# Optimization experiments

Measured on AMD Instinct MI355X. Metric: run time of the kernel, lower is better.

Reference implementation:

```python
import jax, jax.numpy as jnp
import numpy as np

B, N, D_IN, D_HID, D_OUT = 8, 512, 4608, 4608, 1152
DROP = 0.1
INV_SQRT2 = 0.7071067811865476
INV_SQRT_2PI = 0.3989422804014327


def _clean(s):
    # nan -> 1e-5, inf -> 1.0 (matches torch.where chain)
    return jnp.where(jnp.isnan(s), jnp.asarray(1e-5, s.dtype),
                     jnp.where(jnp.isinf(s), jnp.asarray(1.0, s.dtype), s))


def kl_regularizer(w_mu, w_sigma):
    d = w_mu.shape[0]
    ws = jax.nn.softplus(w_sigma)  # log(1+exp(w_sigma))
    return 0.5 * jnp.mean(d * ws + jnp.sum(w_mu * w_mu, axis=0) - d - d * jnp.log(ws))


def vdp_linear(mu_in, Sigma_in, w_mu, w_sigma):
    mu_out = jnp.matmul(mu_in, w_mu)                                 # [B,N,U]
    kl = kl_regularizer(w_mu, w_sigma)
    W_Sigma = jax.nn.softplus(w_sigma)                               # [U]
    Sigma_1 = jnp.matmul(Sigma_in, w_mu * w_mu)                      # w^T Sigma_in w (diag)
    Sigma_2 = jnp.sum(mu_in * mu_in, axis=-1, keepdims=True) * W_Sigma
    Sigma_3 = jnp.sum(Sigma_in, axis=-1, keepdims=True) * W_Sigma
    return mu_out, _clean(Sigma_1 + Sigma_2 + Sigma_3), kl


def vdp_gelu(mu_in, Sigma_in):
    # exact (erf) gelu and its analytic derivative: Phi(x) + x*phi(x)
    cdf = 0.5 * (1.0 + jax.lax.erf(mu_in * INV_SQRT2))
    pdf = jnp.exp(-0.5 * mu_in * mu_in) * INV_SQRT_2PI
    grad = cdf + mu_in * pdf
    return mu_in * cdf, grad * grad * Sigma_in


def vdp_dropout(mu_in, Sigma_in, mask):
    keep = 1.0 - DROP
    m = mask.astype(mu_in.dtype)
    mu_out = mu_in * m / keep                       # torch F.dropout scaling
    Sigma_out = Sigma_in * m / mu_in.shape[-1]      # kept Sigma values (unscaled), / units
    return mu_out, _clean(Sigma_out)


def setup_inputs() -> dict:
    key = jax.random.key(0)
    k = jax.random.split(key, 8)
    mu_in = jax.random.normal(k[0], (B, N, D_IN), dtype=jnp.float32)
    sigma_in = jax.random.uniform(k[1], (B, N, D_IN), dtype=jnp.float32)
    mask1 = jax.random.bernoulli(k[2], 1.0 - DROP, (B, N, D_HID))
    mask2 = jax.random.bernoulli(k[3], 1.0 - DROP, (B, N, D_OUT))
    w_mu1 = 0.05 * jax.random.normal(k[4], (D_IN, D_HID), dtype=jnp.float32)
    w_sigma1 = jnp.full((D_HID,), -4.6, dtype=jnp.float32)
    w_mu2 = 0.05 * jax.random.normal(k[5], (D_HID, D_OUT), dtype=jnp.float32)
    w_sigma2 = jnp.full((D_OUT,), -4.6, dtype=jnp.float32)
    return {"mu_in": mu_in, "sigma_in": sigma_in, "mask1": mask1, "mask2": mask2,
            "w_mu1": w_mu1, "w_sigma1": w_sigma1, "w_mu2": w_mu2, "w_sigma2": w_sigma2}


def reference(mu_in, sigma_in, mask1, mask2, w_mu1, w_sigma1, w_mu2, w_sigma2):
    mu, sig, kl1 = vdp_linear(mu_in, sigma_in, w_mu1, w_sigma1)
    mu, sig = vdp_gelu(mu, sig)
    mu, sig = vdp_dropout(mu, sig, mask1)
    mu, sig, kl2 = vdp_linear(mu, sig, w_mu2, w_sigma2)
    mu, sig = vdp_dropout(mu, sig, mask2)
    return mu, _clean(sig), kl1 + kl2
```

## Files before the change

### kernel.cpp

```cpp
#include <hip/hip_runtime.h>
#include <cstdint>
#include <cstddef>

static constexpr int Mrows = 4096;
static constexpr int K1 = 4608;
static constexpr int N1 = 4608;
static constexpr int N2 = 1152;
static constexpr int SPLITK = 2;
static constexpr int NPART1 = (K1 / 32) * (N1 / 32);
static constexpr int NPART2 = (K1 / 32) * (N2 / 32);

static constexpr float SC_WSQ   = 4096.f;
static constexpr float SC_SIG3  = 16384.f;
static constexpr float DSC_L2   = 1.f / (SC_SIG3 * SC_WSQ);

typedef float  f32x4  __attribute__((ext_vector_type(4)));
typedef __bf16 bf16x8 __attribute__((ext_vector_type(8)));

__device__ __forceinline__ unsigned short f2bf(float f) {
  unsigned int u = __float_as_uint(f);
  u += 0x7fffu + ((u >> 16) & 1u);
  return (unsigned short)(u >> 16);
}
__device__ __forceinline__ float bf2f(unsigned short h) {
  return __uint_as_float(((unsigned int)h) << 16);
}
__device__ __forceinline__ float cleanf(float s) {
  if (__builtin_isnan(s)) return 1e-5f;
  if (__builtin_isinf(s)) return 1.0f;
  return s;
}
__device__ __forceinline__ unsigned int pk_fp8x4(float a, float b, float c, float d) {
  int p = __builtin_amdgcn_cvt_pk_fp8_f32(a, b, 0, false);
  p = __builtin_amdgcn_cvt_pk_fp8_f32(c, d, p, true);
  return (unsigned int)p;
}

__global__ __launch_bounds__(256) void prep_in(
    const float* __restrict__ mu, const float* __restrict__ sg,
    unsigned short* __restrict__ A1, unsigned short* __restrict__ As16,
    float* __restrict__ rmu2, float* __restrict__ rsg)
{
  const int row = blockIdx.x;
  const int tid = threadIdx.x;
  const float4* mup = (const float4*)(mu + (size_t)row * K1);
  const float4* sgp = (const float4*)(sg + (size_t)row * K1);
  ushort4* a1p = (ushort4*)(A1 + (size_t)row * K1);
  ushort4* asp = (ushort4*)(As16 + (size_t)row * K1);
  float smu = 0.f, ssg = 0.f;
  for (int j = tid; j < K1 / 4; j += 256) {
    float4 m4 = mup[j];
    float4 s4 = sgp[j];
    smu += m4.x*m4.x + m4.y*m4.y + m4.z*m4.z + m4.w*m4.w;
    ssg += s4.x + s4.y + s4.z + s4.w;
    a1p[j] = make_ushort4(f2bf(m4.x), f2bf(m4.y), f2bf(m4.z), f2bf(m4.w));
    asp[j] = make_ushort4(f2bf(s4.x), f2bf(s4.y), f2bf(s4.z), f2bf(s4.w));
  }
  __shared__ float red[2][4];
  for (int off = 32; off; off >>= 1) {
    smu += __shfl_down(smu, off);
    ssg += __shfl_down(ssg, off);
  }
  const int lane = tid & 63, wv = tid >> 6;
  if (!lane) { red[0][wv] = smu; red[1][wv] = ssg; }
  __syncthreads();
  if (tid == 0) {
    rmu2[row] = red[0][0] + red[0][1] + red[0][2] + red[0][3];
    rsg[row]  = red[1][0] + red[1][1] + red[1][2] + red[1][3];
  }
}

__global__ __launch_bounds__(256) void prep_w(
    const float* __restrict__ w, unsigned short* __restrict__ Bt,
    void* __restrict__ Bsq, float* __restrict__ partials,
    int K, int N, int sq16)
{
  __shared__ float t[32][33];
  const int kt = blockIdx.x * 32;
  const int nt = blockIdx.y * 32;
  const int tx = threadIdx.x & 31;
  const int ty = threadIdx.x >> 5;
  float loc = 0.f;
#pragma unroll
  for (int i = 0; i < 32; i += 8) {
    float v = w[(size_t)(kt + ty + i) * N + (nt + tx)];
    t[ty + i][tx] = v;
    loc += v * v;
  }
  __syncthreads();
#pragma unroll
  for (int i = 0; i < 32; i += 8) {
    float v = t[tx][ty + i];
    size_t o = (size_t)(nt + ty + i) * K + (kt + tx);
    Bt[o] = f2bf(v);
    if (sq16)
      ((unsigned short*)Bsq)[o] = f2bf(v * v);
    else
      ((unsigned char*)Bsq)[o] =
          (unsigned char)(__builtin_amdgcn_cvt_pk_fp8_f32(v * v * SC_WSQ, 0.f, 0, false) & 0xff);
  }
  __shared__ float red[4];
  for (int off = 32; off; off >>= 1) loc += __shfl_down(loc, off);
  const int lane = threadIdx.x & 63, wv = threadIdx.x >> 6;
  if (!lane) red[wv] = loc;
  __syncthreads();
  if (threadIdx.x == 0)
    partials[blockIdx.y * gridDim.x + blockIdx.x] = red[0] + red[1] + red[2] + red[3];
}

__global__ __launch_bounds__(256) void kl_prep(
    const float* __restrict__ wsig1, const float* __restrict__ wsig2,
    const float* __restrict__ part1, const float* __restrict__ part2,
    float* __restrict__ ws1, float* __restrict__ ws2, float* __restrict__ outkl)
{
  const int tid = threadIdx.x;
  float s1 = 0.f, l1 = 0.f, s2 = 0.f, l2 = 0.f, q1 = 0.f, q2 = 0.f;
  for (int j = tid; j < N1; j += 256) {
    float x = wsig1[j];
    float sp = (x > 20.f) ? x : log1pf(expf(x));
    ws1[j] = sp; s1 += sp; l1 += logf(sp);
  }
  for (int j = tid; j < N2; j += 256) {
    float x = wsig2[j];
    float sp = (x > 20.f) ? x : log1pf(expf(x));
    ws2[j] = sp; s2 += sp; l2 += logf(sp);
  }
  for (int j = tid; j < NPART1; j += 256) q1 += part1[j];
  for (int j = tid; j < NPART2; j += 256) q2 += part2[j];
  __shared__ float red[6][4];
  for (int off = 32; off; off >>= 1) {
    s1 += __shfl_down(s1, off); l1 += __shfl_down(l1, off);
    s2 += __shfl_down(s2, off); l2 += __shfl_down(l2, off);
    q1 += __shfl_down(q1, off); q2 += __shfl_down(q2, off);
  }
  const int lane = tid & 63, wv = tid >> 6;
  if (!lane) {
    red[0][wv] = s1; red[1][wv] = l1; red[2][wv] = s2;
    red[3][wv] = l2; red[4][wv] = q1; red[5][wv] = q2;
  }
  __syncthreads();
  if (tid == 0) {
    float S1v = red[0][0] + red[0][1] + red[0][2] + red[0][3];
    float L1v = red[1][0] + red[1][1] + red[1][2] + red[1][3];
    float S2v = red[2][0] + red[2][1] + red[2][2] + red[2][3];
    float L2v = red[3][0] + red[3][1] + red[3][2] + red[3][3];
    float Q1v = red[4][0] + red[4][1] + red[4][2] + red[4][3];
    float Q2v = red[5][0] + red[5][1] + red[5][2] + red[5][3];
    const float d = 4608.f;
    float kl1 = 0.5f * (d * (S1v / (float)N1) + Q1v / (float)N1 - d - d * (L1v / (float)N1));
    float kl2 = 0.5f * (d * (S2v / (float)N2) + Q2v / (float)N2 - d - d * (L2v / (float)N2));
    outkl[0] = kl1 + kl2;
  }
}

#define GLD16(gp, lp) __builtin_amdgcn_global_load_lds( \
    (__attribute__((address_space(1))) void*)(unsigned short*)(gp), \
    (__attribute__((address_space(3))) void*)(lp), 16, 0, 0)

__global__ __launch_bounds__(512, 2) void gemm256(
    const unsigned short* __restrict__ Amu, const unsigned short* __restrict__ Asg,
    const unsigned short* __restrict__ Bmu, const unsigned short* __restrict__ Bsq,
    unsigned short* __restrict__ Cmu, unsigned short* __restrict__ Csg)
{
  __shared__ __align__(16) char smem[114688];
  char* lA = smem;
  char* lB = smem + 65536;

  const int tid  = threadIdx.x;
  const int lane = tid & 63;
  const int wave = tid >> 6;
  const int which = blockIdx.z;
  const unsigned short* Ag = which ? Asg : Amu;
  const unsigned short* Bg = which ? Bsq : Bmu;
  unsigned short* Cg = which ? Csg : Cmu;

  const int m0 = blockIdx.y * 256;
  const int n0 = blockIdx.x * 192;
  const int wm = (wave >> 2) * 128;
  const int wn = (wave & 3) * 48;
  const int fm = lane & 15;
  const int kq = lane >> 4;

  const int rbase = tid >> 3;
  const int gg = (tid & 7) ^ (rbase & 7);
  const unsigned short* gA0 = Ag + (size_t)(m0 + rbase) * K1 + gg * 8;
  const unsigned short* gB0 = Bg + (size_t)(n0 + rbase) * K1 + gg * 8;

  auto stA = [&](int buf, int h, int kt2) {
    const unsigned short* g = gA0 + (size_t)h * 128 * K1 + (size_t)kt2 * 64;
    char* l = lA + buf * 32768 + h * 16384 + tid * 16;
    GLD16(g, l);
    GLD16(g + (size_t)64 * K1, l + 8192);
  };
  auto stB = [&](int buf, int kt2) {
    const unsigned short* g = gB0 + (size_t)kt2 * 64;
    char* l = lB + buf * 24576 + tid * 16;
    GLD16(g, l);
    GLD16(g + (size_t)64 * K1, l + 8192);
    GLD16(g + (size_t)128 * K1, l + 16384);
  };

  const int abase = (wm + fm) * 128;
  const int bbase = 65536 + (wn + fm) * 128;
  const int x0 = ((0 * 4 + kq) ^ (fm & 7)) * 16;
  const int x1 = ((1 * 4 + kq) ^ (fm & 7)) * 16;

  f32x4 acc[8][3];
#pragma unroll
  for (int i = 0; i < 8; ++i)
#pragma unroll
    for (int j = 0; j < 3; ++j) acc[i][j] = (f32x4){0.f, 0.f, 0.f, 0.f};

  stB(0, 0);
  stA(0, 0, 0); stA(0, 1, 0);
  stB(1, 1);
  asm volatile("s_waitcnt vmcnt(3)" ::: "memory");
  __builtin_amdgcn_s_barrier();

  const int ksteps = K1 / 64;
  for (int kt = 0; kt < ksteps; ++kt) {
    const int cur = kt & 1;
    const char* cA = lA + cur * 32768 + abase;
    const char* cB = smem + cur * 24576 + bbase;

    bf16x8 Af[8][2], Bf[3][2];

#pragma unroll
    for (int j = 0; j < 3; ++j) {
      Bf[j][0] = *(const bf16x8*)(cB + j * 2048 + x0);
      Bf[j][1] = *(const bf16x8*)(cB + j * 2048 + x1);
    }
#pragma unroll
    for (int i = 0; i < 4; ++i) {
      Af[i][0] = *(const bf16x8*)(cA + i * 2048 + x0);
      Af[i][1] = *(const bf16x8*)(cA + i * 2048 + x1);
    }
    if (kt + 1 < ksteps) stA(cur ^ 1, 0, kt + 1);
    asm volatile("s_waitcnt lgkmcnt(8)" ::: "memory");
    __builtin_amdgcn_s_barrier();
    asm volatile("s_waitcnt lgkmcnt(0)" ::: "memory");
    __builtin_amdgcn_s_setprio(1);
#pragma unroll
    for (int i = 0; i < 4; ++i)
#pragma unroll
      for (int j = 0; j < 2; ++j) {
        acc[i][j] = __builtin_amdgcn_mfma_f32_16x16x32_bf16(Af[i][0], Bf[j][0], acc[i][j], 0, 0, 0);
        acc[i][j] = __builtin_amdgcn_mfma_f32_16x16x32_bf16(Af[i][1], Bf[j][1], acc[i][j], 0, 0, 0);
      }
    __builtin_amdgcn_s_setprio(0);
    __builtin_amdgcn_s_barrier();

#pragma unroll
    for (int i = 4; i < 8; ++i) {
      Af[i][0] = *(const bf16x8*)(cA + i * 2048 + x0);
      Af[i][1] = *(const bf16x8*)(cA + i * 2048 + x1);
    }
    if (kt + 1 < ksteps) stA(cur ^ 1, 1, kt + 1);
    __builtin_amdgcn_s_barrier();
    asm volatile("s_waitcnt lgkmcnt(0)" ::: "memory");
    __builtin_amdgcn_s_setprio(1);
#pragma unroll
    for (int i = 4; i < 8; ++i)
#pragma unroll
      for (int j = 0; j < 2; ++j) {
        acc[i][j] = __builtin_amdgcn_mfma_f32_16x16x32_bf16(Af[i][0], Bf[j][0], acc[i][j], 0, 0, 0);
        acc[i][j] = __builtin_amdgcn_mfma_f32_16x16x32_bf16(Af[i][1], Bf[j][1], acc[i][j], 0, 0, 0);
      }
    __builtin_amdgcn_s_setprio(0);
    __builtin_amdgcn_s_barrier();

    if (kt + 2 < ksteps) stB(cur, kt + 2);
    __builtin_amdgcn_s_barrier();
    __builtin_amdgcn_s_setprio(1);
#pragma unroll
    for (int i = 0; i < 8; ++i) {
      acc[i][2] = __builtin_amdgcn_mfma_f32_16x16x32_bf16(Af[i][0], Bf[2][0], acc[i][2], 0, 0, 0);
      acc[i][2] = __builtin_amdgcn_mfma_f32_16x16x32_bf16(Af[i][1], Bf[2][1], acc[i][2], 0, 0, 0);
    }
    __builtin_amdgcn_s_setprio(0);
    if (kt < ksteps - 2) asm volatile("s_waitcnt vmcnt(3)" ::: "memory");
    else                 asm volatile("s_waitcnt vmcnt(0)" ::: "memory");
    __builtin_amdgcn_s_barrier();
  }

  const int rr = (lane >> 4) * 4;
  const int cc = lane & 15;
#pragma unroll
  for (int i = 0; i < 8; ++i) {
    const int grow = m0 + wm + i * 16 + rr;
#pragma unroll
    for (int j = 0; j < 3; ++j) {
      const int gcol = n0 + wn + j * 16 + cc;
      unsigned short* cp = Cg + (size_t)grow * N1 + gcol;
#pragma unroll
      for (int r = 0; r < 4; ++r) cp[(size_t)r * N1] = f2bf(acc[i][j][r]);
    }
  }
}

__device__ __forceinline__ void storeC(float v, float* p) { *p = v; }
__device__ __forceinline__ void storeC(float v, unsigned short* p) { *p = f2bf(v); }

template <typename CT>
__global__ __launch_bounds__(256) void gemm_bt2(
    const unsigned short* __restrict__ Aa, const unsigned char* __restrict__ As8,
    const unsigned short* __restrict__ Ba, const unsigned char* __restrict__ Bq8,
    CT* __restrict__ Ca, CT* __restrict__ Cs,
    int M, int N, int Kstride, int Klen, float sdescale)
{
  __shared__ __align__(16) char smem[32768];
  const int tid = threadIdx.x;
  const int lane = tid & 63;
  const int wave = tid >> 6;

  const int which = blockIdx.z & 1;
  const int slice = blockIdx.z >> 1;

  const int m0 = blockIdx.y * 128;
  const int n0 = blockIdx.x * 128;
  const int wm = (wave & 1) * 64;
  const int wn = (wave >> 1) * 64;

  const int fm = lane & 15;
  const int kq = lane >> 4;

  f32x4 acc[4][4];
#pragma unroll
  for (int i = 0; i < 4; i++)
#pragma unroll
    for (int j = 0; j < 4; j++) acc[i][j] = (f32x4){0.f, 0.f, 0.f, 0.f};

  if (which == 0) {
    const unsigned short* A  = Aa + (size_t)slice * Klen;
    const unsigned short* Bt = Ba + (size_t)slice * Klen;
    unsigned short* lA = (unsigned short*)smem;
    unsigned short* lB = (unsigned short*)(smem + 16384);

    const int c0 = tid, c1 = tid + 256;
    const int r0s = c0 >> 2, k0s = (c0 & 3) ^ ((r0s >> 1) & 3);
    const int r1s = c1 >> 2, k1s = (c1 & 3) ^ ((r1s >> 1) & 3);
    const unsigned short* gA0 = A + (size_t)(m0 + r0s) * Kstride + k0s * 8;
    const unsigned short* gA1 = A + (size_t)(m0 + r1s) * Kstride + k1s * 8;
    const unsigned short* gB0 = Bt + (size_t)(n0 + r0s) * Kstride + k0s * 8;
    const unsigned short* gB1 = Bt + (size_t)(n0 + r1s) * Kstride + k1s * 8;

    int aoff[4], boff[4];
#pragma unroll
    for (int i = 0; i < 4; i++) {
      int ra = wm + i * 16 + fm;
      aoff[i] = ra * 32 + ((kq ^ ((ra >> 1) & 3)) * 8);
      int rb = wn + i * 16 + fm;
      boff[i] = rb * 32 + ((kq ^ ((rb >> 1) & 3)) * 8);
    }

    GLD16(gA0, &lA[c0 * 8]); GLD16(gA1, &lA[c1 * 8]);
    GLD16(gB0, &lB[c0 * 8]); GLD16(gB1, &lB[c1 * 8]);
    gA0 += 32; gA1 += 32; gB0 += 32; gB1 += 32;

    const int ksteps = Klen >> 5;
    int cur = 0;
    for (int kt = 0; kt < ksteps; kt++) {
      __syncthreads();
      if (kt + 1 < ksteps) {
        const int nb = cur ^ 1;
        GLD16(gA0, &lA[nb * 4096 + c0 * 8]); GLD16(gA1, &lA[nb * 4096 + c1 * 8]);
        GLD16(gB0, &lB[nb * 4096 + c0 * 8]); GLD16(gB1, &lB[nb * 4096 + c1 * 8]);
        gA0 += 32; gA1 += 32; gB0 += 32; gB1 += 32;
      }
      bf16x8 af[4], bfr[4];
#pragma unroll
      for (int i = 0; i < 4; i++) af[i] = *(const bf16x8*)&lA[cur * 4096 + aoff[i]];
#pragma unroll
      for (int i = 0; i < 4; i++) bfr[i] = *(const bf16x8*)&lB[cur * 4096 + boff[i]];
#pragma unroll
      for (int i = 0; i < 4; i++)
#pragma unroll
        for (int j = 0; j < 4; j++)
          acc[i][j] = __builtin_amdgcn_mfma_f32_16x16x32_bf16(af[i], bfr[j], acc[i][j], 0, 0, 0);
      cur ^= 1;
    }

    CT* C = Ca + (size_t)slice * M * N;
    const int rr = (lane >> 4) * 4;
    const int cc = lane & 15;
#pragma unroll
    for (int i = 0; i < 4; i++) {
      const int grow = m0 + wm + i * 16 + rr;
#pragma unroll
      for (int j = 0; j < 4; j++) {
        const int gcol = n0 + wn + j * 16 + cc;
        CT* cp = C + (size_t)grow * N + gcol;
#pragma unroll
        for (int r = 0; r < 4; r++) storeC(acc[i][j][r], cp + (size_t)r * N);
      }
    }
  } else {
    const unsigned char* A  = As8 + (size_t)slice * Klen;
    const unsigned char* Bt = Bq8 + (size_t)slice * Klen;
    char* lA = smem;
    char* lB = smem + 16384;

    const int s1 = tid, s2 = tid + 256;
    const int r1 = s1 & 127, h1 = s1 >> 7;
    const int r2 = s2 & 127, h2 = s2 >> 7;
    const unsigned char* gA0 = A + (size_t)(m0 + r1) * Kstride + h1 * 16;
    const unsigned char* gA1 = A + (size_t)(m0 + r2) * Kstride + h2 * 16;
    const unsigned char* gB0 = Bt + (size_t)(n0 + r1) * Kstride + h1 * 16;
    const unsigned char* gB1 = Bt + (size_t)(n0 + r2) * Kstride + h2 * 16;

    int aoff8[2][4], boff8[2][4];
#pragma unroll
    for (int hh = 0; hh < 2; hh++)
#pragma unroll
      for (int i = 0; i < 4; i++) {
        const int c = hh * 4 + kq;
        aoff8[hh][i] = (c >> 1) * 2048 + (wm + i * 16 + fm) * 16 + (c & 1) * 8;
        boff8[hh][i] = (c >> 1) * 2048 + (wn + i * 16 + fm) * 16 + (c & 1) * 8;
      }

    GLD16(gA0, lA + s1 * 16); GLD16(gA1, lA + s2 * 16);
    GLD16(gB0, lB + s1 * 16); GLD16(gB1, lB + s2 * 16);
    gA0 += 64; gA1 += 64; gB0 += 64; gB1 += 64;

    const int ksteps = Klen >> 6;
    int cur = 0;
    for (int kt = 0; kt < ksteps; kt++) {
      __syncthreads();
      if (kt + 1 < ksteps) {
        const int nb = cur ^ 1;
        GLD16(gA0, lA + nb * 8192 + s1 * 16); GLD16(gA1, lA + nb * 8192 + s2 * 16);
        GLD16(gB0, lB + nb * 8192 + s1 * 16); GLD16(gB1, lB + nb * 8192 + s2 * 16);
        gA0 += 64; gA1 += 64; gB0 += 64; gB1 += 64;
      }
#pragma unroll
      for (int hh = 0; hh < 2; hh++) {
        long av[4], bv[4];
#pragma unroll
        for (int i = 0; i < 4; i++) av[i] = *(const long*)(lA + cur * 8192 + aoff8[hh][i]);
#pragma unroll
        for (int i = 0; i < 4; i++) bv[i] = *(const long*)(lB + cur * 8192 + boff8[hh][i]);
#pragma unroll
        for (int i = 0; i < 4; i++)
#pragma unroll
          for (int j = 0; j < 4; j++)
            acc[i][j] = __builtin_amdgcn_mfma_f32_16x16x32_fp8_fp8(av[i], bv[j], acc[i][j], 0, 0, 0);
      }
      cur ^= 1;
    }

    CT* C = Cs + (size_t)slice * M * N;
    const int rr = (lane >> 4) * 4;
    const int cc = lane & 15;
#pragma unroll
    for (int i = 0; i < 4; i++) {
      const int grow = m0 + wm + i * 16 + rr;
#pragma unroll
      for (int j = 0; j < 4; j++) {
        const int gcol = n0 + wn + j * 16 + cc;
        CT* cp = C + (size_t)grow * N + gcol;
#pragma unroll
        for (int r = 0; r < 4; r++) storeC(acc[i][j][r] * sdescale, cp + (size_t)r * N);
      }
    }
  }
}

__global__ __launch_bounds__(256) void mid_kernel(
    const unsigned short* __restrict__ mu1, const unsigned short* __restrict__ S1,
    const int* __restrict__ mask1, const float* __restrict__ ws1,
    const float* __restrict__ rmu2, const float* __restrict__ rsg,
    unsigned short* __restrict__ A2, unsigned char* __restrict__ As2,
    float* __restrict__ r2mu, float* __restrict__ r2sg)
{
  const int row = blockIdx.x;
  const int tid = threadIdx.x;
  const float rterm = rmu2[row] + rsg[row];
  const ushort4* mup = (const ushort4*)(mu1 + (size_t)row * N1);
  const ushort4* s1p = (const ushort4*)(S1 + (size_t)row * N1);
  const int4* mkp = (const int4*)(mask1 + (size_t)row * N1);
  const float4* wsp = (const float4*)ws1;
  ushort4* a2p = (ushort4*)(A2 + (size_t)row * N1);
  unsigned int* as2p = (unsigned int*)(As2 + (size_t)row * N1);
  float smu = 0.f, ssg = 0.f;
  for (int j = tid; j < N1 / 4; j += 256) {
    ushort4 m4 = mup[j]; ushort4 s4 = s1p[j]; int4 k4 = mkp[j]; float4 w4 = wsp[j];
    float xv[4] = {bf2f(m4.x), bf2f(m4.y), bf2f(m4.z), bf2f(m4.w)};
    float Sv[4] = {bf2f(s4.x), bf2f(s4.y), bf2f(s4.z), bf2f(s4.w)};
    float wv[4] = {w4.x, w4.y, w4.z, w4.w};
    int   kv[4] = {k4.x, k4.y, k4.z, k4.w};
    unsigned short oa[4];
    float os[4];
#pragma unroll
    for (int t = 0; t < 4; t++) {
      float sig1 = cleanf(Sv[t] + rterm * wv[t]);
      float x = xv[t];
      float cdf = 0.5f * (1.f + erff(x * 0.70710678118654752f));
      float pdf = expf(-0.5f * x * x) * 0.3989422804014327f;
      float g = cdf + x * pdf;
      float mu2v = x * cdf;
      float sig2 = g * g * sig1;
      float mm = (float)kv[t];
      float mu3 = mu2v * mm * (1.f / 0.9f);
      float sig3 = cleanf(sig2 * mm * (1.f / 4608.f));
      smu += mu3 * mu3;
      ssg += sig3;
      oa[t] = f2bf(mu3);
      os[t] = sig3 * SC_SIG3;
    }
    a2p[j] = make_ushort4(oa[0], oa[1], oa[2], oa[3]);
    as2p[j] = pk_fp8x4(os[0], os[1], os[2], os[3]);
  }
  __shared__ float red[2][4];
  for (int off = 32; off; off >>= 1) {
    smu += __shfl_down(smu, off);
    ssg += __shfl_down(ssg, off);
  }
  const int lane = tid & 63, wv2 = tid >> 6;
  if (!lane) { red[0][wv2] = smu; red[1][wv2] = ssg; }
  __syncthreads();
  if (tid == 0) {
    r2mu[row] = red[0][0] + red[0][1] + red[0][2] + red[0][3];
    r2sg[row] = red[1][0] + red[1][1] + red[1][2] + red[1][3];
  }
}

__global__ __launch_bounds__(256) void final_kernel(
    const float* __restrict__ pmu, const float* __restrict__ psig,
    const int* __restrict__ mask2, const float* __restrict__ ws2,
    const float* __restrict__ r2mu, const float* __restrict__ r2sg,
    float* __restrict__ out_mu, float* __restrict__ out_sig)
{
  const int row = blockIdx.x;
  const int tid = threadIdx.x;
  const float rterm = r2mu[row] + r2sg[row];
  const size_t sstride = (size_t)Mrows * N2;
  const float4* mup0 = (const float4*)(pmu + (size_t)row * N2);
  const float4* sbp0 = (const float4*)(psig + (size_t)row * N2);
  const int4* mkp = (const int4*)(mask2 + (size_t)row * N2);
  const float4* wsp = (const float4*)ws2;
  float4* omp = (float4*)(out_mu + (size_t)row * N2);
  float4* osp = (float4*)(out_sig + (size_t)row * N2);
  const size_t s4 = sstride / 4;
  for (int j = tid; j < N2 / 4; j += 256) {
    float4 m4 = mup0[j];
    float4 sb = sbp0[j];
#pragma unroll
    for (int s = 1; s < SPLITK; s++) {
      float4 a = mup0[j + s * s4];
      float4 b = sbp0[j + s * s4];
      m4.x += a.x; m4.y += a.y; m4.z += a.z; m4.w += a.w;
      sb.x += b.x; sb.y += b.y; sb.z += b.z; sb.w += b.w;
    }
    int4 k4 = mkp[j]; float4 w4 = wsp[j];
    float mo[4], so[4];
    float mv[4] = {m4.x, m4.y, m4.z, m4.w};
    float sv[4] = {sb.x, sb.y, sb.z, sb.w};
    float wv[4] = {w4.x, w4.y, w4.z, w4.w};
    int   kv[4] = {k4.x, k4.y, k4.z, k4.w};
#pragma unroll
    for (int t = 0; t < 4; t++) {
      float sig4 = cleanf(sv[t] + rterm * wv[t]);
      float mm = (float)kv[t];
      float mu5 = mv[t] * mm * (1.f / 0.9f);
      float sig5 = cleanf(sig4 * mm * (1.f / 1152.f));
      mo[t] = mu5;
      so[t] = cleanf(sig5);
    }
    omp[j] = make_float4(mo[0], mo[1], mo[2], mo[3]);
    osp[j] = make_float4(so[0], so[1], so[2], so[3]);
  }
}

extern "C" void kernel_launch(void* const* d_in, const int* in_sizes, int n_in,
                              void* d_out, int out_size, void* d_ws, size_t ws_size,
                              hipStream_t stream)
{
  const float* mu_in = (const float*)d_in[0];
  const float* sg_in = (const float*)d_in[1];
  const int* mask1 = (const int*)d_in[2];
  const int* mask2 = (const int*)d_in[3];
  const float* w_mu1 = (const float*)d_in[4];
  const float* wsig1 = (const float*)d_in[5];
  const float* w_mu2 = (const float*)d_in[6];
  const float* wsig2 = (const float*)d_in[7];
  float* out = (float*)d_out;

  char* ws = (char*)d_ws;
  const size_t oA1  = 0;
  const size_t oAs  = oA1  + (size_t)37748736;
  const size_t oB1t = oAs  + (size_t)37748736;
  const size_t oB1q = oB1t + (size_t)42467328;
  const size_t oB2t = oB1q + (size_t)42467328;
  const size_t oB2q = oB2t + (size_t)10616832;
  const size_t oMu1 = oB2q + (size_t)10616832;
  const size_t oS1  = oMu1 + (size_t)37748736;
  const size_t oVec = oS1  + (size_t)37748736;

  unsigned short* A1     = (unsigned short*)(ws + oA1);
  unsigned short* As16   = (unsigned short*)(ws + oAs);
  unsigned char*  As8    = (unsigned char*)(ws + oAs);
  unsigned short* B1t    = (unsigned short*)(ws + oB1t);
  unsigned short* B1sq16 = (unsigned short*)(ws + oB1q);
  unsigned short* B2t    = (unsigned short*)(ws + oB2t);
  unsigned char*  B2q8   = (unsigned char*)(ws + oB2q);
  unsigned short* mu1b   = (unsigned short*)(ws + oMu1);
  unsigned short* S1b16  = (unsigned short*)(ws + oS1);
  float* pmu  = (float*)(ws + oB1t);
  float* psig = (float*)(ws + oMu1);

  float* rmu2 = (float*)(ws + oVec);
  float* rsg  = rmu2 + Mrows;
  float* r2mu = rsg + Mrows;
  float* r2sg = r2mu + Mrows;
  float* ws1v = r2sg + Mrows;
  float* ws2v = ws1v + N1;
  float* part1 = ws2v + N2;
  float* part2 = part1 + NPART1;

  prep_in<<<Mrows, 256, 0, stream>>>(mu_in, sg_in, A1, As16, rmu2, rsg);
  prep_w<<<dim3(K1 / 32, N1 / 32), 256, 0, stream>>>(w_mu1, B1t, (void*)B1sq16, part1, K1, N1, 1);
  prep_w<<<dim3(K1 / 32, N2 / 32), 256, 0, stream>>>(w_mu2, B2t, (void*)B2q8, part2, K1, N2, 0);
  kl_prep<<<1, 256, 0, stream>>>(wsig1, wsig2, part1, part2, ws1v, ws2v,
                                 out + (size_t)2 * Mrows * N2);

  gemm256<<<dim3(N1 / 192, Mrows / 256, 2), 512, 0, stream>>>(
      A1, As16, B1t, B1sq16, mu1b, S1b16);

  mid_kernel<<<Mrows, 256, 0, stream>>>(mu1b, S1b16, mask1, ws1v, rmu2, rsg,
                                        A1, As8, r2mu, r2sg);

  gemm_bt2<float><<<dim3(N2 / 128, Mrows / 128, 2 * SPLITK), 256, 0, stream>>>(
      A1, As8, B2t, B2q8, pmu, psig, Mrows, N2, K1, K1 / SPLITK, DSC_L2);

  final_kernel<<<Mrows, 256, 0, stream>>>(pmu, psig, mask2, ws2v, r2mu, r2sg,
                                          out, out + (size_t)Mrows * N2);
  (void)in_sizes; (void)n_in; (void)out_size; (void)ws_size;
}
```

Measured before the change: 879.4 us.

## Reuse the large 256x192 bf16 GEMM for layer 2, dropping the fp8 split-K kernel

Layer 2 now runs through the templated 256x192 pipelined bf16 GEMM (templated on output width and type) instead of a separate 128x128 split-K kernel whose sigma path used fp8. The sigma activations and squared weights for layer 2 are stored as bf16 rather than scaled fp8, and the split-K partial sums are no longer added in the final kernel. This trades the cheaper fp8 MFMA and smaller operands for a better-pipelined kernel with no partial-sum traffic. It gives only 6x16x2 = 192 blocks for layer 2, which may leave the GPU underused.

```diff
diff --git a/kernel.cpp b/kernel.cpp
--- a/kernel.cpp
+++ b/kernel.cpp
@@ -6,13 +6,8 @@
 static constexpr int K1 = 4608;
 static constexpr int N1 = 4608;
 static constexpr int N2 = 1152;
-static constexpr int SPLITK = 2;
 static constexpr int NPART1 = (K1 / 32) * (N1 / 32);
 static constexpr int NPART2 = (K1 / 32) * (N2 / 32);
-
-static constexpr float SC_WSQ   = 4096.f;
-static constexpr float SC_SIG3  = 16384.f;
-static constexpr float DSC_L2   = 1.f / (SC_SIG3 * SC_WSQ);
 
 typedef float  f32x4  __attribute__((ext_vector_type(4)));
 typedef __bf16 bf16x8 __attribute__((ext_vector_type(8)));
@@ -29,11 +24,6 @@
   if (__builtin_isnan(s)) return 1e-5f;
   if (__builtin_isinf(s)) return 1.0f;
   return s;
-}
-__device__ __forceinline__ unsigned int pk_fp8x4(float a, float b, float c, float d) {
-  int p = __builtin_amdgcn_cvt_pk_fp8_f32(a, b, 0, false);
-  p = __builtin_amdgcn_cvt_pk_fp8_f32(c, d, p, true);
-  return (unsigned int)p;
 }
 
 __global__ __launch_bounds__(256) void prep_in(
@@ -72,8 +62,8 @@
 
 __global__ __launch_bounds__(256) void prep_w(
     const float* __restrict__ w, unsigned short* __restrict__ Bt,
-    void* __restrict__ Bsq, float* __restrict__ partials,
-    int K, int N, int sq16)
+    unsigned short* __restrict__ Bsq, float* __restrict__ partials,
+    int K, int N)
 {
   __shared__ float t[32][33];
   const int kt = blockIdx.x * 32;
@@ -92,12 +82,8 @@
   for (int i = 0; i < 32; i += 8) {
     float v = t[tx][ty + i];
     size_t o = (size_t)(nt + ty + i) * K + (kt + tx);
-    Bt[o] = f2bf(v);
-    if (sq16)
-      ((unsigned short*)Bsq)[o] = f2bf(v * v);
-    else
-      ((unsigned char*)Bsq)[o] =
-          (unsigned char)(__builtin_amdgcn_cvt_pk_fp8_f32(v * v * SC_WSQ, 0.f, 0, false) & 0xff);
+    Bt[o]  = f2bf(v);
+    Bsq[o] = f2bf(v * v);
   }
   __shared__ float red[4];
   for (int off = 32; off; off >>= 1) loc += __shfl_down(loc, off);
@@ -157,10 +143,14 @@
     (__attribute__((address_space(1))) void*)(unsigned short*)(gp), \
     (__attribute__((address_space(3))) void*)(lp), 16, 0, 0)
 
+__device__ __forceinline__ void storeC(float v, float* p) { *p = v; }
+__device__ __forceinline__ void storeC(float v, unsigned short* p) { *p = f2bf(v); }
+
+template <int NT, typename CT>
 __global__ __launch_bounds__(512, 2) void gemm256(
     const unsigned short* __restrict__ Amu, const unsigned short* __restrict__ Asg,
     const unsigned short* __restrict__ Bmu, const unsigned short* __restrict__ Bsq,
-    unsigned short* __restrict__ Cmu, unsigned short* __restrict__ Csg)
+    CT* __restrict__ Cmu, CT* __restrict__ Csg)
 {
   __shared__ __align__(16) char smem[114688];
   char* lA = smem;
@@ -172,7 +162,7 @@
   const int which = blockIdx.z;
   const unsigned short* Ag = which ? Asg : Amu;
   const unsigned short* Bg = which ? Bsq : Bmu;
-  unsigned short* Cg = which ? Csg : Cmu;
+  CT* Cg = which ? Csg : Cmu;
 
   const int m0 = blockIdx.y * 256;
   const int n0 = blockIdx.x * 192;
@@ -291,176 +281,9 @@
 #pragma unroll
     for (int j = 0; j < 3; ++j) {
       const int gcol = n0 + wn + j * 16 + cc;
-      unsigned short* cp = Cg + (size_t)grow * N1 + gcol;
-#pragma unroll
-      for (int r = 0; r < 4; ++r) cp[(size_t)r * N1] = f2bf(acc[i][j][r]);
-    }
-  }
-}
-
-__device__ __forceinline__ void storeC(float v, float* p) { *p = v; }
-__device__ __forceinline__ void storeC(float v, unsigned short* p) { *p = f2bf(v); }
-
-template <typename CT>
-__global__ __launch_bounds__(256) void gemm_bt2(
-    const unsigned short* __restrict__ Aa, const unsigned char* __restrict__ As8,
-    const unsigned short* __restrict__ Ba, const unsigned char* __restrict__ Bq8,
-    CT* __restrict__ Ca, CT* __restrict__ Cs,
-    int M, int N, int Kstride, int Klen, float sdescale)
-{
-  __shared__ __align__(16) char smem[32768];
-  const int tid = threadIdx.x;
-  const int lane = tid & 63;
-  const int wave = tid >> 6;
-
-  const int which = blockIdx.z & 1;
-  const int slice = blockIdx.z >> 1;
-
-  const int m0 = blockIdx.y * 128;
-  const int n0 = blockIdx.x * 128;
-  const int wm = (wave & 1) * 64;
-  const int wn = (wave >> 1) * 64;
-
-  const int fm = lane & 15;
-  const int kq = lane >> 4;
-
-  f32x4 acc[4][4];
-#pragma unroll
-  for (int i = 0; i < 4; i++)
-#pragma unroll
-    for (int j = 0; j < 4; j++) acc[i][j] = (f32x4){0.f, 0.f, 0.f, 0.f};
-
-  if (which == 0) {
-    const unsigned short* A  = Aa + (size_t)slice * Klen;
-    const unsigned short* Bt = Ba + (size_t)slice * Klen;
-    unsigned short* lA = (unsigned short*)smem;
-    unsigned short* lB = (unsigned short*)(smem + 16384);
-
-    const int c0 = tid, c1 = tid + 256;
-    const int r0s = c0 >> 2, k0s = (c0 & 3) ^ ((r0s >> 1) & 3);
-    const int r1s = c1 >> 2, k1s = (c1 & 3) ^ ((r1s >> 1) & 3);
-    const unsigned short* gA0 = A + (size_t)(m0 + r0s) * Kstride + k0s * 8;
-    const unsigned short* gA1 = A + (size_t)(m0 + r1s) * Kstride + k1s * 8;
-    const unsigned short* gB0 = Bt + (size_t)(n0 + r0s) * Kstride + k0s * 8;
-    const unsigned short* gB1 = Bt + (size_t)(n0 + r1s) * Kstride + k1s * 8;
-
-    int aoff[4], boff[4];
-#pragma unroll
-    for (int i = 0; i < 4; i++) {
-      int ra = wm + i * 16 + fm;
-      aoff[i] = ra * 32 + ((kq ^ ((ra >> 1) & 3)) * 8);
-      int rb = wn + i * 16 + fm;
-      boff[i] = rb * 32 + ((kq ^ ((rb >> 1) & 3)) * 8);
-    }
-
-    GLD16(gA0, &lA[c0 * 8]); GLD16(gA1, &lA[c1 * 8]);
-    GLD16(gB0, &lB[c0 * 8]); GLD16(gB1, &lB[c1 * 8]);
-    gA0 += 32; gA1 += 32; gB0 += 32; gB1 += 32;
-
-    const int ksteps = Klen >> 5;
-    int cur = 0;
-    for (int kt = 0; kt < ksteps; kt++) {
-      __syncthreads();
-      if (kt + 1 < ksteps) {
-        const int nb = cur ^ 1;
-        GLD16(gA0, &lA[nb * 4096 + c0 * 8]); GLD16(gA1, &lA[nb * 4096 + c1 * 8]);
-        GLD16(gB0, &lB[nb * 4096 + c0 * 8]); GLD16(gB1, &lB[nb * 4096 + c1 * 8]);
-        gA0 += 32; gA1 += 32; gB0 += 32; gB1 += 32;
-      }
-      bf16x8 af[4], bfr[4];
-#pragma unroll
-      for (int i = 0; i < 4; i++) af[i] = *(const bf16x8*)&lA[cur * 4096 + aoff[i]];
-#pragma unroll
-      for (int i = 0; i < 4; i++) bfr[i] = *(const bf16x8*)&lB[cur * 4096 + boff[i]];
-#pragma unroll
-      for (int i = 0; i < 4; i++)
-#pragma unroll
-        for (int j = 0; j < 4; j++)
-          acc[i][j] = __builtin_amdgcn_mfma_f32_16x16x32_bf16(af[i], bfr[j], acc[i][j], 0, 0, 0);
-      cur ^= 1;
-    }
-
-    CT* C = Ca + (size_t)slice * M * N;
-    const int rr = (lane >> 4) * 4;
-    const int cc = lane & 15;
-#pragma unroll
-    for (int i = 0; i < 4; i++) {
-      const int grow = m0 + wm + i * 16 + rr;
-#pragma unroll
-      for (int j = 0; j < 4; j++) {
-        const int gcol = n0 + wn + j * 16 + cc;
-        CT* cp = C + (size_t)grow * N + gcol;
-#pragma unroll
-        for (int r = 0; r < 4; r++) storeC(acc[i][j][r], cp + (size_t)r * N);
-      }
-    }
-  } else {
-    const unsigned char* A  = As8 + (size_t)slice * Klen;
-    const unsigned char* Bt = Bq8 + (size_t)slice * Klen;
-    char* lA = smem;
-    char* lB = smem + 16384;
-
-    const int s1 = tid, s2 = tid + 256;
-    const int r1 = s1 & 127, h1 = s1 >> 7;
-    const int r2 = s2 & 127, h2 = s2 >> 7;
-    const unsigned char* gA0 = A + (size_t)(m0 + r1) * Kstride + h1 * 16;
-    const unsigned char* gA1 = A + (size_t)(m0 + r2) * Kstride + h2 * 16;
-    const unsigned char* gB0 = Bt + (size_t)(n0 + r1) * Kstride + h1 * 16;
-    const unsigned char* gB1 = Bt + (size_t)(n0 + r2) * Kstride + h2 * 16;
-
-    int aoff8[2][4], boff8[2][4];
-#pragma unroll
-    for (int hh = 0; hh < 2; hh++)
-#pragma unroll
-      for (int i = 0; i < 4; i++) {
-        const int c = hh * 4 + kq;
-        aoff8[hh][i] = (c >> 1) * 2048 + (wm + i * 16 + fm) * 16 + (c & 1) * 8;
-        boff8[hh][i] = (c >> 1) * 2048 + (wn + i * 16 + fm) * 16 + (c & 1) * 8;
-      }
-
-    GLD16(gA0, lA + s1 * 16); GLD16(gA1, lA + s2 * 16);
-    GLD16(gB0, lB + s1 * 16); GLD16(gB1, lB + s2 * 16);
-    gA0 += 64; gA1 += 64; gB0 += 64; gB1 += 64;
-
-    const int ksteps = Klen >> 6;
-    int cur = 0;
-    for (int kt = 0; kt < ksteps; kt++) {
-      __syncthreads();
-      if (kt + 1 < ksteps) {
-        const int nb = cur ^ 1;
-        GLD16(gA0, lA + nb * 8192 + s1 * 16); GLD16(gA1, lA + nb * 8192 + s2 * 16);
-        GLD16(gB0, lB + nb * 8192 + s1 * 16); GLD16(gB1, lB + nb * 8192 + s2 * 16);
-        gA0 += 64; gA1 += 64; gB0 += 64; gB1 += 64;
-      }
-#pragma unroll
-      for (int hh = 0; hh < 2; hh++) {
-        long av[4], bv[4];
-#pragma unroll
-        for (int i = 0; i < 4; i++) av[i] = *(const long*)(lA + cur * 8192 + aoff8[hh][i]);
-#pragma unroll
-        for (int i = 0; i < 4; i++) bv[i] = *(const long*)(lB + cur * 8192 + boff8[hh][i]);
-#pragma unroll
-        for (int i = 0; i < 4; i++)
-#pragma unroll
-          for (int j = 0; j < 4; j++)
-            acc[i][j] = __builtin_amdgcn_mfma_f32_16x16x32_fp8_fp8(av[i], bv[j], acc[i][j], 0, 0, 0);
-      }
-      cur ^= 1;
-    }
-
-    CT* C = Cs + (size_t)slice * M * N;
-    const int rr = (lane >> 4) * 4;
-    const int cc = lane & 15;
-#pragma unroll
-    for (int i = 0; i < 4; i++) {
-      const int grow = m0 + wm + i * 16 + rr;
-#pragma unroll
-      for (int j = 0; j < 4; j++) {
-        const int gcol = n0 + wn + j * 16 + cc;
-        CT* cp = C + (size_t)grow * N + gcol;
-#pragma unroll
-        for (int r = 0; r < 4; r++) storeC(acc[i][j][r] * sdescale, cp + (size_t)r * N);
-      }
+      CT* cp = Cg + (size_t)grow * NT + gcol;
+#pragma unroll
+      for (int r = 0; r < 4; ++r) storeC(acc[i][j][r], cp + (size_t)r * NT);
     }
   }
 }
@@ -469,7 +292,7 @@
     const unsigned short* __restrict__ mu1, const unsigned short* __restrict__ S1,
     const int* __restrict__ mask1, const float* __restrict__ ws1,
     const float* __restrict__ rmu2, const float* __restrict__ rsg,
-    unsigned short* __restrict__ A2, unsigned char* __restrict__ As2,
+    unsigned short* __restrict__ A2, unsigned short* __restrict__ As2,
     float* __restrict__ r2mu, float* __restrict__ r2sg)
 {
   const int row = blockIdx.x;
@@ -480,7 +303,7 @@
   const int4* mkp = (const int4*)(mask1 + (size_t)row * N1);
   const float4* wsp = (const float4*)ws1;
   ushort4* a2p = (ushort4*)(A2 + (size_t)row * N1);
-  unsigned int* as2p = (unsigned int*)(As2 + (size_t)row * N1);
+  ushort4* as2p = (ushort4*)(As2 + (size_t)row * N1);
   float smu = 0.f, ssg = 0.f;
   for (int j = tid; j < N1 / 4; j += 256) {
     ushort4 m4 = mup[j]; ushort4 s4 = s1p[j]; int4 k4 = mkp[j]; float4 w4 = wsp[j];
@@ -488,8 +311,7 @@
     float Sv[4] = {bf2f(s4.x), bf2f(s4.y), bf2f(s4.z), bf2f(s4.w)};
     float wv[4] = {w4.x, w4.y, w4.z, w4.w};
     int   kv[4] = {k4.x, k4.y, k4.z, k4.w};
-    unsigned short oa[4];
-    float os[4];
+    unsigned short oa[4], os[4];
 #pragma unroll
     for (int t = 0; t < 4; t++) {
       float sig1 = cleanf(Sv[t] + rterm * wv[t]);
@@ -505,10 +327,10 @@
       smu += mu3 * mu3;
       ssg += sig3;
       oa[t] = f2bf(mu3);
-      os[t] = sig3 * SC_SIG3;
+      os[t] = f2bf(sig3);
     }
     a2p[j] = make_ushort4(oa[0], oa[1], oa[2], oa[3]);
-    as2p[j] = pk_fp8x4(os[0], os[1], os[2], os[3]);
+    as2p[j] = make_ushort4(os[0], os[1], os[2], os[3]);
   }
   __shared__ float red[2][4];
   for (int off = 32; off; off >>= 1) {
@@ -533,24 +355,15 @@
   const int row = blockIdx.x;
   const int tid = threadIdx.x;
   const float rterm = r2mu[row] + r2sg[row];
-  const size_t sstride = (size_t)Mrows * N2;
   const float4* mup0 = (const float4*)(pmu + (size_t)row * N2);
   const float4* sbp0 = (const float4*)(psig + (size_t)row * N2);
   const int4* mkp = (const int4*)(mask2 + (size_t)row * N2);
   const float4* wsp = (const float4*)ws2;
   float4* omp = (float4*)(out_mu + (size_t)row * N2);
   float4* osp = (float4*)(out_sig + (size_t)row * N2);
-  const size_t s4 = sstride / 4;
   for (int j = tid; j < N2 / 4; j += 256) {
     float4 m4 = mup0[j];
     float4 sb = sbp0[j];
-#pragma unroll
-    for (int s = 1; s < SPLITK; s++) {
-      float4 a = mup0[j + s * s4];
-      float4 b = sbp0[j + s * s4];
-      m4.x += a.x; m4.y += a.y; m4.z += a.z; m4.w += a.w;
-      sb.x += b.x; sb.y += b.y; sb.z += b.z; sb.w += b.w;
-    }
     int4 k4 = mkp[j]; float4 w4 = wsp[j];
     float mo[4], so[4];
     float mv[4] = {m4.x, m4.y, m4.z, m4.w};
@@ -598,11 +411,10 @@
 
   unsigned short* A1     = (unsigned short*)(ws + oA1);
   unsigned short* As16   = (unsigned short*)(ws + oAs);
-  unsigned char*  As8    = (unsigned char*)(ws + oAs);
   unsigned short* B1t    = (unsigned short*)(ws + oB1t);
   unsigned short* B1sq16 = (unsigned short*)(ws + oB1q);
   unsigned short* B2t    = (unsigned short*)(ws + oB2t);
-  unsigned char*  B2q8   = (unsigned char*)(ws + oB2q);
+  unsigned short* B2sq16 = (unsigned short*)(ws + oB2q);
   unsigned short* mu1b   = (unsigned short*)(ws + oMu1);
   unsigned short* S1b16  = (unsigned short*)(ws + oS1);
   float* pmu  = (float*)(ws + oB1t);
@@ -618,19 +430,19 @@
   float* part2 = part1 + NPART1;
 
   prep_in<<<Mrows, 256, 0, stream>>>(mu_in, sg_in, A1, As16, rmu2, rsg);
-  prep_w<<<dim3(K1 / 32, N1 / 32), 256, 0, stream>>>(w_mu1, B1t, (void*)B1sq16, part1, K1, N1, 1);
-  prep_w<<<dim3(K1 / 32, N2 / 32), 256, 0, stream>>>(w_mu2, B2t, (void*)B2q8, part2, K1, N2, 0);
+  prep_w<<<dim3(K1 / 32, N1 / 32), 256, 0, stream>>>(w_mu1, B1t, B1sq16, part1, K1, N1);
+  prep_w<<<dim3(K1 / 32, N2 / 32), 256, 0, stream>>>(w_mu2, B2t, B2sq16, part2, K1, N2);
   kl_prep<<<1, 256, 0, stream>>>(wsig1, wsig2, part1, part2, ws1v, ws2v,
                                  out + (size_t)2 * Mrows * N2);
 
-  gemm256<<<dim3(N1 / 192, Mrows / 256, 2), 512, 0, stream>>>(
+  gemm256<N1, unsigned short><<<dim3(N1 / 192, Mrows / 256, 2), 512, 0, stream>>>(
       A1, As16, B1t, B1sq16, mu1b, S1b16);
 
   mid_kernel<<<Mrows, 256, 0, stream>>>(mu1b, S1b16, mask1, ws1v, rmu2, rsg,
-                                        A1, As8, r2mu, r2sg);
-
-  gemm_bt2<float><<<dim3(N2 / 128, Mrows / 128, 2 * SPLITK), 256, 0, stream>>>(
-      A1, As8, B2t, B2q8, pmu, psig, Mrows, N2, K1, K1 / SPLITK, DSC_L2);
+                                        A1, As16, r2mu, r2sg);
+
+  gemm256<N2, float><<<dim3(N2 / 192, Mrows / 256, 2), 512, 0, stream>>>(
+      A1, As16, B2t, B2sq16, pmu, psig);
 
   final_kernel<<<Mrows, 256, 0, stream>>>(pmu, psig, mask2, ws2v, r2mu, r2sg,
                                           out, out + (size_t)Mrows * N2);
```

Measured after the change: 826.7 us. -6.0%, faster.
